# Kernel tuning notes

Measured on AMD Instinct MI355X. Metric: run time of the kernel, lower is better.

## Reference

```python
import jax, jax.numpy as jnp
import numpy as np

B = 4096      # batch
D = 256       # flattened input feature dim
NUMFEAT = 1 + D + D * (D + 1) // 2  # 33153: bias + linear + quadratic terms


def setup_inputs() -> dict:
    key = jax.random.key(0)
    k1, k2 = jax.random.split(key)
    x = jax.random.normal(k1, (B, D), dtype=jnp.float32)
    # nn.Linear(numfeat, 10, bias=False): weight shape (10, numfeat)
    W = jax.random.normal(k2, (10, NUMFEAT), dtype=jnp.float32) * 0.01
    return {"x": x, "W": W}


def reference(x, W):
    # x: (B, D) -- original does x.view(B, -1); already 2D here.
    b, d = x.shape
    # sklearn PolynomialFeatures(degree=2) column order:
    # [1, x_0..x_{d-1}, x_0*x_0, x_0*x_1, ..., x_{d-1}*x_{d-1}]
    # i.e. combinations_with_replacement == upper-triangular (incl. diagonal)
    iu0, iu1 = np.triu_indices(d)  # static index constants
    ones = jnp.ones((b, 1), dtype=x.dtype)
    cross = x[:, iu0] * x[:, iu1]          # (B, D*(D+1)/2)
    feats = jnp.concatenate([ones, x, cross], axis=1)  # (B, NUMFEAT)
    return feats @ W.T                      # (B, 10)
```

## Files before the change

kernel.cpp:

```cpp
#include <hip/hip_runtime.h>


#define DD 256
#define NF 33153
#define TPB 256
#define ASTRIDE 264

typedef __attribute__((ext_vector_type(8))) short short8;
typedef __attribute__((ext_vector_type(4))) float floatx4;
typedef __attribute__((ext_vector_type(4), aligned(4))) float float4a;

union S8U { unsigned u[4]; short8 s; };

__device__ inline unsigned pack2(float lo, float hi) {
    unsigned a = __builtin_bit_cast(unsigned, hi) + 0x8000u;
    unsigned b = __builtin_bit_cast(unsigned, lo) + 0x8000u;
    return __builtin_amdgcn_perm(a, b, 0x07060302u);
}

__global__ __launch_bounds__(TPB)
void gbuild_kernel(const float* __restrict__ W, unsigned short* __restrict__ G) {
    int oi = blockIdx.x * 8 + (threadIdx.x >> 5);
    int c0 = (threadIdx.x & 31) * 8;
    int o = oi >> 8, i = oi & 255;
    int base = o * NF + 257 + i * 255 - ((i * (i - 1)) >> 1);
    float4a w0 = *(const float4a*)&W[base + c0];
    float4a w1 = *(const float4a*)&W[base + c0 + 4];
    float f[8] = {w0.x, w0.y, w0.z, w0.w, w1.x, w1.y, w1.z, w1.w};
#pragma unroll
    for (int e = 0; e < 8; ++e)
        if (c0 + e < i) f[e] = 0.f;
    S8U p;
    p.u[0] = pack2(f[0], f[1]); p.u[1] = pack2(f[2], f[3]);
    p.u[2] = pack2(f[4], f[5]); p.u[3] = pack2(f[6], f[7]);
    *(short8*)&G[oi * DD + c0] = p.s;
}

__global__ __launch_bounds__(TPB, 3)
void PolynomialRegression_75385265979710_kernel(const float* __restrict__ x,
                                                const float* __restrict__ W,
                                                const unsigned short* __restrict__ G,
                                                float* __restrict__ out) {
    __shared__ __align__(16) unsigned short As[64 * ASTRIDE];
    __shared__ float red[4 * 64];

    const int tid  = threadIdx.x;
    const int lane = tid & 63, wave = tid >> 6;
    const int ln   = lane & 15, quad = lane >> 4;
    const int q8   = quad * 8;
    const int rowbase = blockIdx.x * 64;
    const int o  = blockIdx.y;
    const int g1 = wave, g2 = 7 - wave;
    const int rem = 8 - wave;

#pragma unroll
    for (int it = 0; it < 8; ++it) {
        int idx = it * 2048 + tid * 8;
        int r = idx >> 8, c = idx & 255;
        const float* src = &x[(rowbase + r) * DD + c];
        float4a v0 = *(const float4a*)src;
        float4a v1 = *(const float4a*)(src + 4);
        S8U p;
        p.u[0] = pack2(v0.x, v0.y); p.u[1] = pack2(v0.z, v0.w);
        p.u[2] = pack2(v1.x, v1.y); p.u[3] = pack2(v1.z, v1.w);
        *(short8*)&As[r * ASTRIDE + c] = p.s;
    }

    int iRow[4];
    float w1v[4];
#pragma unroll
    for (int nt = 0; nt < 4; ++nt) {
        int g = (nt < 2) ? g1 : g2;
        iRow[nt] = g * 32 + (nt & 1) * 16 + ln;
        w1v[nt]  = W[o * NF + 1 + iRow[nt]];
    }
    const float bias = W[o * NF];

    __syncthreads();

    floatx4 acc[4][4];
#pragma unroll
    for (int mt = 0; mt < 4; ++mt)
#pragma unroll
        for (int nt = 0; nt < 4; ++nt) acc[mt][nt] = (floatx4)0.f;

    const unsigned short* Gy = G + (o * DD) * DD;

#pragma unroll
    for (int t = 0; t < 9; ++t) {
        const bool first = (t < rem);
        const int g  = first ? g1 : g2;
        const int kc = first ? (g1 + t) : (g2 + (t - rem));
        const unsigned short* gb = Gy + (g * 32 + ln) * DD + kc * 32 + q8;
        short8 b0 = *(const short8*)gb;
        short8 b1 = *(const short8*)(gb + 16 * DD);
        short8 a[4];
#pragma unroll
        for (int mt = 0; mt < 4; ++mt)
            a[mt] = *(const short8*)&As[(mt * 16 + ln) * ASTRIDE + kc * 32 + q8];
        if (first) {
#pragma unroll
            for (int mt = 0; mt < 4; ++mt) {
                acc[mt][0] = __builtin_amdgcn_mfma_f32_16x16x32_bf16(a[mt], b0, acc[mt][0], 0, 0, 0);
                acc[mt][1] = __builtin_amdgcn_mfma_f32_16x16x32_bf16(a[mt], b1, acc[mt][1], 0, 0, 0);
            }
        } else {
#pragma unroll
            for (int mt = 0; mt < 4; ++mt) {
                acc[mt][2] = __builtin_amdgcn_mfma_f32_16x16x32_bf16(a[mt], b0, acc[mt][2], 0, 0, 0);
                acc[mt][3] = __builtin_amdgcn_mfma_f32_16x16x32_bf16(a[mt], b1, acc[mt][3], 0, 0, 0);
            }
        }
    }

#pragma unroll
    for (int mt = 0; mt < 4; ++mt) {
#pragma unroll
        for (int r = 0; r < 4; ++r) {
            const int m = mt * 16 + quad * 4 + r;
            float p = 0.f;
#pragma unroll
            for (int nt = 0; nt < 4; ++nt) {
                unsigned u = As[m * ASTRIDE + iRow[nt]];
                float xv = __builtin_bit_cast(float, u << 16);
                p = fmaf(xv, acc[mt][nt][r] + w1v[nt], p);
            }
            p += __shfl_xor(p, 1);
            p += __shfl_xor(p, 2);
            p += __shfl_xor(p, 4);
            p += __shfl_xor(p, 8);
            if (ln == 0) red[wave * 64 + m] = p;
        }
    }
    __syncthreads();

    if (tid < 64) {
        float s = red[tid] + red[64 + tid] + red[128 + tid] + red[192 + tid]
                + bias;
        out[(rowbase + tid) * 10 + o] = s;
    }
}

extern "C" void kernel_launch(void* const* d_in, const int* in_sizes, int n_in,
                              void* d_out, int out_size, void* d_ws, size_t ws_size,
                              hipStream_t stream) {
    const float* x = (const float*)d_in[0];
    const float* W = (const float*)d_in[1];
    float* out = (float*)d_out;

    unsigned short* G = (unsigned short*)d_ws;

    gbuild_kernel<<<2560 / 8, TPB, 0, stream>>>(W, G);

    dim3 grid(4096 / 64, 10);
    PolynomialRegression_75385265979710_kernel<<<grid, TPB, 0, stream>>>(x, W, G, out);
}
```

Before: 69.33 us.

## Fuse bf16 weight-matrix build into main kernel, reading triangular W directly

Removes the separate gbuild kernel that wrote a bf16 dense upper-triangular matrix G to workspace. The main kernel now loads fp32 weights straight from the packed triangular layout of W, converts them to bf16 in registers, and masks the diagonal-tile lower entries with bitmasks. This saves one kernel launch and a global round trip through G. In exchange every block does the fp32 loads and conversion redundantly, roughly doubling B-operand load bytes, and the per-row float4 loads may be unaligned.

```diff
diff --git a/kernel.cpp b/kernel.cpp
--- a/kernel.cpp
+++ b/kernel.cpp
@@ -18,28 +18,20 @@
     return __builtin_amdgcn_perm(a, b, 0x07060302u);
 }
 
-__global__ __launch_bounds__(TPB)
-void gbuild_kernel(const float* __restrict__ W, unsigned short* __restrict__ G) {
-    int oi = blockIdx.x * 8 + (threadIdx.x >> 5);
-    int c0 = (threadIdx.x & 31) * 8;
-    int o = oi >> 8, i = oi & 255;
-    int base = o * NF + 257 + i * 255 - ((i * (i - 1)) >> 1);
-    float4a w0 = *(const float4a*)&W[base + c0];
-    float4a w1 = *(const float4a*)&W[base + c0 + 4];
-    float f[8] = {w0.x, w0.y, w0.z, w0.w, w1.x, w1.y, w1.z, w1.w};
-#pragma unroll
-    for (int e = 0; e < 8; ++e)
-        if (c0 + e < i) f[e] = 0.f;
-    S8U p;
-    p.u[0] = pack2(f[0], f[1]); p.u[1] = pack2(f[2], f[3]);
-    p.u[2] = pack2(f[4], f[5]); p.u[3] = pack2(f[6], f[7]);
-    *(short8*)&G[oi * DD + c0] = p.s;
+__device__ inline short8 load_pack8(const float* __restrict__ p) {
+    float4a v0 = *(const float4a*)p;
+    float4a v1 = *(const float4a*)(p + 4);
+    S8U r;
+    r.u[0] = pack2(v0.x, v0.y); r.u[1] = pack2(v0.z, v0.w);
+    r.u[2] = pack2(v1.x, v1.y); r.u[3] = pack2(v1.z, v1.w);
+    return r.s;
 }
+
+__device__ inline int troff(int i) { return 257 + 255 * i - ((i * (i - 1)) >> 1); }
 
 __global__ __launch_bounds__(TPB, 3)
 void PolynomialRegression_75385265979710_kernel(const float* __restrict__ x,
                                                 const float* __restrict__ W,
-                                                const unsigned short* __restrict__ G,
                                                 float* __restrict__ out) {
     __shared__ __align__(16) unsigned short As[64 * ASTRIDE];
     __shared__ float red[4 * 64];
@@ -66,15 +58,35 @@
         *(short8*)&As[r * ASTRIDE + c] = p.s;
     }
 
+    const float* __restrict__ Wo = W + o * NF;
+
+    const int offA0 = troff(g1 * 32 + ln)      + q8;
+    const int offA1 = troff(g1 * 32 + 16 + ln) + q8;
+    const int offB0 = troff(g2 * 32 + ln)      + q8;
+    const int offB1 = troff(g2 * 32 + 16 + ln) + q8;
+
+    unsigned mA[4], mB[4];
+#pragma unroll
+    for (int w2 = 0; w2 < 4; ++w2) {
+        mA[w2] = ((q8 + 2 * w2     < ln) ? 0u : 0x0000FFFFu)
+               | ((q8 + 2 * w2 + 1 < ln) ? 0u : 0xFFFF0000u);
+        mB[w2] = ((q8 + 2 * w2     < 16 + ln) ? 0u : 0x0000FFFFu)
+               | ((q8 + 2 * w2 + 1 < 16 + ln) ? 0u : 0xFFFF0000u);
+    }
+
     int iRow[4];
     float w1v[4];
 #pragma unroll
     for (int nt = 0; nt < 4; ++nt) {
         int g = (nt < 2) ? g1 : g2;
         iRow[nt] = g * 32 + (nt & 1) * 16 + ln;
-        w1v[nt]  = W[o * NF + 1 + iRow[nt]];
+        w1v[nt]  = Wo[1 + iRow[nt]];
     }
-    const float bias = W[o * NF];
+    const float bias = Wo[0];
+
+    S8U pb0, pb1;
+    pb0.s = load_pack8(Wo + offA0 + g1 * 32);
+    pb1.s = load_pack8(Wo + offA1 + g1 * 32);
 
     __syncthreads();
 
@@ -84,31 +96,37 @@
 #pragma unroll
         for (int nt = 0; nt < 4; ++nt) acc[mt][nt] = (floatx4)0.f;
 
-    const unsigned short* Gy = G + (o * DD) * DD;
-
 #pragma unroll
     for (int t = 0; t < 9; ++t) {
         const bool first = (t < rem);
-        const int g  = first ? g1 : g2;
         const int kc = first ? (g1 + t) : (g2 + (t - rem));
-        const unsigned short* gb = Gy + (g * 32 + ln) * DD + kc * 32 + q8;
-        short8 b0 = *(const short8*)gb;
-        short8 b1 = *(const short8*)(gb + 16 * DD);
+        const int co = kc * 32;
+        S8U b0, b1;
+        if (t == 0) {
+            b0 = pb0; b1 = pb1;
+        } else {
+            b0.s = load_pack8(Wo + (first ? offA0 : offB0) + co);
+            b1.s = load_pack8(Wo + (first ? offA1 : offB1) + co);
+        }
+        if (t == 0 || t == rem) {
+#pragma unroll
+            for (int w2 = 0; w2 < 4; ++w2) { b0.u[w2] &= mA[w2]; b1.u[w2] &= mB[w2]; }
+        }
         short8 a[4];
 #pragma unroll
         for (int mt = 0; mt < 4; ++mt)
-            a[mt] = *(const short8*)&As[(mt * 16 + ln) * ASTRIDE + kc * 32 + q8];
+            a[mt] = *(const short8*)&As[(mt * 16 + ln) * ASTRIDE + co + q8];
         if (first) {
 #pragma unroll
             for (int mt = 0; mt < 4; ++mt) {
-                acc[mt][0] = __builtin_amdgcn_mfma_f32_16x16x32_bf16(a[mt], b0, acc[mt][0], 0, 0, 0);
-                acc[mt][1] = __builtin_amdgcn_mfma_f32_16x16x32_bf16(a[mt], b1, acc[mt][1], 0, 0, 0);
+                acc[mt][0] = __builtin_amdgcn_mfma_f32_16x16x32_bf16(a[mt], b0.s, acc[mt][0], 0, 0, 0);
+                acc[mt][1] = __builtin_amdgcn_mfma_f32_16x16x32_bf16(a[mt], b1.s, acc[mt][1], 0, 0, 0);
             }
         } else {
 #pragma unroll
             for (int mt = 0; mt < 4; ++mt) {
-                acc[mt][2] = __builtin_amdgcn_mfma_f32_16x16x32_bf16(a[mt], b0, acc[mt][2], 0, 0, 0);
-                acc[mt][3] = __builtin_amdgcn_mfma_f32_16x16x32_bf16(a[mt], b1, acc[mt][3], 0, 0, 0);
+                acc[mt][2] = __builtin_amdgcn_mfma_f32_16x16x32_bf16(a[mt], b0.s, acc[mt][2], 0, 0, 0);
+                acc[mt][3] = __builtin_amdgcn_mfma_f32_16x16x32_bf16(a[mt], b1.s, acc[mt][3], 0, 0, 0);
             }
         }
     }
@@ -148,10 +166,6 @@
     const float* W = (const float*)d_in[1];
     float* out = (float*)d_out;
 
-    unsigned short* G = (unsigned short*)d_ws;
-
-    gbuild_kernel<<<2560 / 8, TPB, 0, stream>>>(W, G);
-
     dim3 grid(4096 / 64, 10);
-    PolynomialRegression_75385265979710_kernel<<<grid, TPB, 0, stream>>>(x, W, G, out);
+    PolynomialRegression_75385265979710_kernel<<<grid, TPB, 0, stream>>>(x, W, out);
 }
```

Result: no change. 69.78 us (+0.6%).
